# Optimization experiments

Hardware: AMD Instinct MI355X
Metric: run time of the kernel (lower is better)

Reference implementation:

```python
import jax, jax.numpy as jnp
import numpy as np

B, C, Hf, Wf = 32, 512, 16, 16
S = Hf * Wf            # 256 kv tokens
D = 2048               # d_model
DIN = 512              # d_input (attention embed dim)
HEADS = 8
DH = DIN // HEADS
T = 50                 # iterations (internal ticks)
M = 25                 # memory_length
HH = 16                # memory_hidden_dims
NSA = 512              # n_synch_action
NSO = 512              # n_synch_out
OUT = 1000             # out_dims


def _ln(x, g, b, eps=1e-5):
    mu = x.mean(-1, keepdims=True)
    var = ((x - mu) ** 2).mean(-1, keepdims=True)
    return (x - mu) / jnp.sqrt(var + eps) * g + b


def _glu(x):
    a, b = jnp.split(x, 2, axis=-1)
    return a * jax.nn.sigmoid(b)


def setup_inputs() -> dict:
    key = jax.random.key(0)
    ki = iter(jax.random.split(key, 40))
    def rn(shape, s=0.02):
        return jax.random.normal(next(ki), shape, jnp.float32) * s
    inp = {}
    inp['x'] = jax.random.normal(next(ki), (B, C, Hf, Wf), jnp.float32)
    # kv_proj: Linear(C->DIN) + LayerNorm
    inp['kv_w'] = rn((C, DIN)); inp['kv_b'] = jnp.zeros((DIN,), jnp.float32)
    inp['ln_kv_g'] = jnp.ones((DIN,), jnp.float32); inp['ln_kv_b'] = jnp.zeros((DIN,), jnp.float32)
    # q_proj: Linear(NSA->DIN)
    inp['q_w'] = rn((NSA, DIN)); inp['q_b'] = jnp.zeros((DIN,), jnp.float32)
    # MultiheadAttention projections
    inp['Wq'] = rn((DIN, DIN)); inp['bq'] = jnp.zeros((DIN,), jnp.float32)
    inp['Wk'] = rn((DIN, DIN)); inp['bk'] = jnp.zeros((DIN,), jnp.float32)
    inp['Wv'] = rn((DIN, DIN)); inp['bv'] = jnp.zeros((DIN,), jnp.float32)
    inp['Wo'] = rn((DIN, DIN)); inp['bo'] = jnp.zeros((DIN,), jnp.float32)
    # synapse: Linear(DIN+D -> 2D) + GLU + LayerNorm(D)
    inp['syn_w'] = rn((DIN + D, 2 * D)); inp['syn_b'] = jnp.zeros((2 * D,), jnp.float32)
    inp['ln_syn_g'] = jnp.ones((D,), jnp.float32); inp['ln_syn_b'] = jnp.zeros((D,), jnp.float32)
    # per-neuron NLMs (SuperLinear weights: (in,out,N))
    inp['nlm_w1'] = rn((M, 2 * HH, D), 0.1); inp['nlm_b1'] = jnp.zeros((1, D, 2 * HH), jnp.float32)
    inp['nlm_w2'] = rn((HH, 2, D), 0.1); inp['nlm_b2'] = jnp.zeros((1, D, 2), jnp.float32)
    # output projector
    inp['out_w'] = rn((NSO, OUT)); inp['out_b'] = jnp.zeros((OUT,), jnp.float32)
    # learnable decay params (clamped to [0,15] in forward)
    inp['decay_action'] = jax.random.uniform(next(ki), (NSA,), jnp.float32)
    inp['decay_out'] = jax.random.uniform(next(ki), (NSO,), jnp.float32)
    # learned start state
    inp['start_trace'] = rn((D, M), 0.05)
    inp['start_act'] = rn((D,), 0.05)
    # random-pairing neuron indices (fixed at init in the original)
    inp['idx_la'] = jax.random.randint(next(ki), (NSA,), 0, D)
    inp['idx_ra'] = jax.random.randint(next(ki), (NSA,), 0, D)
    inp['idx_lo'] = jax.random.randint(next(ki), (NSO,), 0, D)
    inp['idx_ro'] = jax.random.randint(next(ki), (NSO,), 0, D)
    return inp


def reference(x, kv_w, kv_b, ln_kv_g, ln_kv_b, q_w, q_b, Wq, bq, Wk, bk, Wv, bv, Wo, bo,
              syn_w, syn_b, ln_syn_g, ln_syn_b, nlm_w1, nlm_b1, nlm_w2, nlm_b2,
              out_w, out_b, decay_action, decay_out, start_trace, start_act,
              idx_la, idx_ra, idx_lo, idx_ro):
    # featurise: identity backbone, flatten spatial to tokens, project to DIN
    feats = x.reshape(B, C, S).transpose(0, 2, 1)                 # (B,S,C)
    kv = _ln(feats @ kv_w + kv_b, ln_kv_g, ln_kv_b)               # (B,S,DIN)
    kh = (kv @ Wk + bk).reshape(B, S, HEADS, DH).transpose(0, 2, 1, 3)  # (B,H,S,DH)
    vh = (kv @ Wv + bv).reshape(B, S, HEADS, DH).transpose(0, 2, 1, 3)
    r_a = jnp.exp(-jnp.clip(decay_action, 0.0, 15.0))[None]       # (1,NSA)
    r_o = jnp.exp(-jnp.clip(decay_out, 0.0, 15.0))[None]          # (1,NSO)

    def nlm(trace):  # per-neuron MLP over the memory axis: (B,D,M) -> (B,D)
        h = _glu(jnp.einsum('bdm,mhd->bdh', trace, nlm_w1) + nlm_b1)
        return _glu(jnp.einsum('bdh,hod->bdo', h, nlm_w2) + nlm_b2)[..., 0]

    act0 = jnp.broadcast_to(start_act[None], (B, D))
    trace0 = jnp.broadcast_to(start_trace[None], (B, D, M))
    # out-synchronisation initialised from the start state (before the loop)
    a_o0 = act0[:, idx_lo] * act0[:, idx_ro]
    b_o0 = jnp.ones_like(a_o0)
    a_a0 = jnp.zeros((B, NSA), jnp.float32)
    b_a0 = jnp.zeros((B, NSA), jnp.float32)
    log_out = jnp.log(jnp.float32(OUT))
    scale = 1.0 / jnp.sqrt(jnp.float32(DH))

    def step(carry, _):
        trace, act, a_a, b_a, a_o, b_o = carry
        # action synchronisation (decayed pairwise products, sync = alpha/sqrt(beta))
        a_a = r_a * a_a + act[:, idx_la] * act[:, idx_ra]
        b_a = r_a * b_a + 1.0
        sync_a = a_a / jnp.sqrt(b_a)
        # attention readout (single query token)
        q = sync_a @ q_w + q_b                                    # (B,DIN)
        qh = (q @ Wq + bq).reshape(B, HEADS, 1, DH)
        attn = jax.nn.softmax(jnp.einsum('bhqd,bhkd->bhqk', qh, kh) * scale, -1)
        o = jnp.einsum('bhqk,bhkd->bhqd', attn, vh).transpose(0, 2, 1, 3).reshape(B, DIN)
        attn_out = o @ Wo + bo
        # synapse MLP -> new pre-activation state
        pre = jnp.concatenate([attn_out, act], axis=-1)           # (B,DIN+D)
        state = _ln(_glu(pre @ syn_w + syn_b), ln_syn_g, ln_syn_b)
        trace = jnp.concatenate([trace[:, :, 1:], state[:, :, None]], axis=-1)
        act = nlm(trace)                                          # (B,D)
        # output synchronisation + prediction
        a_o = r_o * a_o + act[:, idx_lo] * act[:, idx_ro]
        b_o = r_o * b_o + 1.0
        sync_o = a_o / jnp.sqrt(b_o)
        pred = sync_o @ out_w + out_b                             # (B,OUT)
        logp = jax.nn.log_softmax(pred, -1)
        ne = -(jnp.exp(logp) * logp).sum(-1) / log_out
        cert = jnp.stack([ne, 1.0 - ne], axis=-1)                 # (B,2)
        return (trace, act, a_a, b_a, a_o, b_o), (pred, cert, sync_o)

    _, (preds, certs, syncs) = jax.lax.scan(step, (trace0, act0, a_a0, b_a0, a_o0, b_o0), None, length=T)
    predictions = jnp.transpose(preds, (1, 2, 0))                 # (B,OUT,T)
    certainties = jnp.transpose(certs, (1, 2, 0))                 # (B,2,T)
    return predictions, certainties, syncs[-1]
```

## Files before the change

kernel.cpp:

```cpp
#include <hip/hip_runtime.h>
#include <math.h>

#define BB 32
#define CC 512
#define SS 256
#define DD 2048
#define DIN 512
#define NH 8
#define DHD 64
#define TT 50
#define MM 25
#define HHID 16
#define NSA 512
#define NSO 512
#define NOUT 1000

__global__ void init_kernel(const float* __restrict__ dec_a, const float* __restrict__ dec_o,
                            const float* __restrict__ start_act, const float* __restrict__ start_trace,
                            const int* __restrict__ idx_lo, const int* __restrict__ idx_ro,
                            float* __restrict__ r_a, float* __restrict__ r_o,
                            float* __restrict__ a_a, float* __restrict__ b_a,
                            float* __restrict__ a_o, float* __restrict__ b_o,
                            float* __restrict__ trace)
{
    int i = blockIdx.x * 256 + threadIdx.x;
    if (i < 512) {
        r_a[i] = expf(-fminf(fmaxf(dec_a[i], 0.f), 15.f));
        r_o[i] = expf(-fminf(fmaxf(dec_o[i], 0.f), 15.f));
    }
    if (i < BB * NSA) {
        a_a[i] = 0.f; b_a[i] = 0.f;
        int j = i & 511;
        a_o[i] = start_act[idx_lo[j]] * start_act[idx_ro[j]];
        b_o[i] = 1.f;
    }
    if (i < BB * MM * DD) {
        int rem = i % (MM * DD);
        int m = rem / DD, d = rem % DD;
        trace[i] = start_trace[d * MM + m];
    }
}

template<int AMODE, int SMODE>
__global__ void gemm64(const float* __restrict__ A, const float* __restrict__ Bm,
                       const float* __restrict__ bias, float* __restrict__ Cm,
                       int Mdim, int Ndim, int Kdim)
{
    __shared__ float As[16 * 65];
    __shared__ float Bs[16 * 64];
    int row0 = blockIdx.x * 64;
    int col0 = blockIdx.y * 64;
    int t = threadIdx.x;
    int tx = t & 15, ty = t >> 4;
    float acc[4][4] = {};
    for (int k0 = 0; k0 < Kdim; k0 += 16) {
        if (AMODE == 0) {
            for (int i = t; i < 1024; i += 256) {
                int kk = i & 15, r = i >> 4;
                As[kk * 65 + r] = A[(size_t)(row0 + r) * Kdim + k0 + kk];
            }
        } else {
            int b = row0 / SS, s0 = row0 % SS;
            for (int i = t; i < 1024; i += 256) {
                int r = i & 63, kk = i >> 6;
// ... 46 lines not shown
    float v1 = buf[(size_t)row * 512 + 256 + t];
    red[t] = v0 + v1; __syncthreads();
    for (int off = 128; off; off >>= 1) { if (t < off) red[t] += red[t + off]; __syncthreads(); }
    float mu = red[0] * (1.f / 512.f); __syncthreads();
    float d0 = v0 - mu, d1 = v1 - mu;
    red[t] = d0 * d0 + d1 * d1; __syncthreads();
    for (int off = 128; off; off >>= 1) { if (t < off) red[t] += red[t + off]; __syncthreads(); }
    float rstd = 1.f / sqrtf(red[0] * (1.f / 512.f) + 1e-5f);
    buf[(size_t)row * 512 + t]       = d0 * rstd * g[t] + bta[t];
    buf[(size_t)row * 512 + 256 + t] = d1 * rstd * g[t + 256] + bta[t + 256];
}

__global__ void bqq_kernel(const float* __restrict__ q_b, const float* __restrict__ Wq,
                           const float* __restrict__ bq, float* __restrict__ bqq)
{
    int c = blockIdx.x * 256 + threadIdx.x;
    if (c >= 512) return;
    float acc = bq[c];
    for (int k = 0; k < 512; k++) acc += q_b[k] * Wq[k * 512 + c];
    bqq[c] = acc;
}

__global__ void bias2_kernel(const float* __restrict__ bo, const float* __restrict__ syn_w,
                             const float* __restrict__ syn_b, float* __restrict__ bias2)
{
    int c = blockIdx.x * 256 + threadIdx.x;
    if (c >= 4096) return;
    float acc = syn_b[c];
    for (int k = 0; k < 512; k++) acc += bo[k] * syn_w[(size_t)k * 4096 + c];
    bias2[c] = acc;
}

__global__ void wt_build(const float* __restrict__ W2, const float* __restrict__ syn_w,
                         float* __restrict__ WT)
{
    __shared__ float tile[32][33];
    int k0 = blockIdx.x * 32, c0 = blockIdx.y * 32;
    int t = threadIdx.x;
    int col = t & 31, rq = t >> 5;
    #pragma unroll
    for (int q = 0; q < 4; ++q) {
        int kk = q * 8 + rq;
        int k = k0 + kk;
        const float* src = (k < 512 ? W2 : syn_w) + (size_t)k * 4096 + c0;
        tile[kk][col] = src[col];
    }
    __syncthreads();
    #pragma unroll
    for (int q = 0; q < 4; ++q) {
        int cc = q * 8 + rq;
        WT[(size_t)(c0 + cc) * 2560 + k0 + col] = tile[col][cc];
    }
}

__global__ void act0_kernel(const float* __restrict__ start_act, float* __restrict__ act0slot)
{
    int i = blockIdx.x * 256 + threadIdx.x;
    if (i < BB * DD) act0slot[i] = start_act[i & (DD - 1)];
}

__global__ void pad_outw(const float* __restrict__ out_w, const float* __restrict__ out_b,
                         float* __restrict__ out_wp, float* __restrict__ out_bp)
{
    int i = blockIdx.x * 256 + threadIdx.x;
    if (i < 512 * 1024) {
        int r = i >> 10, c = i & 1023;
        out_wp[i] = (c < 1000) ? out_w[r * 1000 + c] : 0.f;
    }
    if (i < 1024) out_bp[i] = (i < 1000) ? out_b[i] : 0.f;
}

__global__ __launch_bounds__(256) void k1_front(
    const float* __restrict__ act, const int* __restrict__ la, const int* __restrict__ ra,
    const float* __restrict__ r_a,
    const float* __restrict__ aold, const float* __restrict__ bold,
    float* __restrict__ anew, float* __restrict__ bnew,
    const float* __restrict__ Wqq, const float* __restrict__ bqq,
    const float* __restrict__ khT, const float* __restrict__ vh,
    float* __restrict__ obuf)
{
    __shared__ float sa[512];
    __shared__ float qp[256];
    __shared__ float qs[64];
    __shared__ float ps[256];
    __shared__ float red[256];
    int bh = blockIdx.x, b = bh >> 3, h = bh & 7;
    int tid = threadIdx.x;
    const float* actb = act + b * DD;
    for (int j = tid; j < 512; j += 256) {
        float p = actb[la[j]] * actb[ra[j]];
        float r = r_a[j];
        float aa = r * aold[b * 512 + j] + p;
        float bb = r * bold[b * 512 + j] + 1.f;
        sa[j] = aa / sqrtf(bb);
        if (h == 0) { anew[b * 512 + j] = aa; bnew[b * 512 + j] = bb; }
    }
    __syncthreads();
    {
        int cl = tid & 63, q = tid >> 6;
        const float* wcol = Wqq + h * 64 + cl;
        float acc = 0.f;
        #pragma unroll 8
        for (int k = q * 128; k < q * 128 + 128; ++k)
            acc += sa[k] * wcol[k * 512];
        qp[tid] = acc;
    }
    __syncthreads();
    if (tid < 64)
        qs[tid] = qp[tid] + qp[tid + 64] + qp[tid + 128] + qp[tid + 192] + bqq[h * 64 + tid];
    __syncthreads();
    const float* kb = khT + (size_t)bh * 64 * 256;
    float sc = 0.f;
    #pragma unroll 8
    for (int dh = 0; dh < 64; ++dh) sc += qs[dh] * kb[dh * 256 + tid];
    sc *= 0.125f;
    red[tid] = sc; __syncthreads();
    for (int off = 128; off; off >>= 1) { if (tid < off) red[tid] = fmaxf(red[tid], red[tid + off]); __syncthreads(); }
    float mx = red[0]; __syncthreads();
    float e = expf(sc - mx);
    red[tid] = e; __syncthreads();
    for (int off = 128; off; off >>= 1) { if (tid < off) red[tid] += red[tid + off]; __syncthreads(); }
    float inv = 1.f / red[0];
    ps[tid] = e * inv;
    __syncthreads();
    int dh = tid & 63, ch = tid >> 6;
    const float* vb = vh + (size_t)bh * 256 * 64;
    float acc = 0.f;
    for (int s = ch * 64; s < ch * 64 + 64; ++s) acc += ps[s] * vb[s * 64 + dh];
    red[tid] = acc; __syncthreads();
    if (tid < 128) red[tid] += red[tid + 128];
    __syncthreads();
    if (tid < 64) obuf[b * 512 + h * 64 + tid] = red[tid] + red[tid + 64];
}

__global__ __launch_bounds__(256) void k2_glu(
    const float* __restrict__ obuf, const float* __restrict__ act,
    const float* __restrict__ WT, const float* __restrict__ bias2,
    float* __restrict__ glbufT, float* __restrict__ partials)
{
    __shared__ float As[2 * 32 * 160];
    int tid = threadIdx.x, blk = blockIdx.x;
    int kh = tid >> 7;
    int cpair = (tid >> 5) & 3;
    int r = tid & 31;
    int c = blk * 4 + cpair;
    const float* wta = WT + (size_t)c * 2560 + kh * 1280;
    const float* wtb = WT + (size_t)(c + 2048) * 2560 + kh * 1280;
    float acc_a = 0.f, acc_b = 0.f;
    for (int ri = 0; ri < 8; ++ri) {
        __syncthreads();
        #pragma unroll
        for (int q = 0; q < 10; ++q) {
            int i = tid + q * 256;
            int hh = i / 1280;
            int rem = i - hh * 1280;
            int rr = rem / 40, kg = rem - (rem / 40) * 40;
            int k = hh * 1280 + ri * 160 + kg * 4;
            float4 v;
            if (k < 512) v = *(const float4*)(obuf + rr * 512 + k);
            else         v = *(const float4*)(act + rr * 2048 + (k - 512));
            *(float4*)(As + hh * 5120 + rr * 160 + ((kg ^ (rr & 7)) << 2)) = v;
        }
        __syncthreads();
        const float* Ar = As + kh * 5120 + r * 160;
        const float* wtaa = wta + ri * 160;
        const float* wtbb = wtb + ri * 160;
        int sw = r & 7;
        #pragma unroll 8
        for (int kc = 0; kc < 40; ++kc) {
            float4 a4 = *(const float4*)(Ar + ((kc ^ sw) << 2));
            float4 wa = *(const float4*)(wtaa + kc * 4);
            float4 wb = *(const float4*)(wtbb + kc * 4);
            acc_a += a4.x * wa.x + a4.y * wa.y + a4.z * wa.z + a4.w * wa.w;
            acc_b += a4.x * wb.x + a4.y * wb.y + a4.z * wb.z + a4.w * wb.w;
        }
    }
    __syncthreads();
    float* red_a = As;
    float* red_b = As + 128;
    float* gls   = As + 256;
    float* gl2s  = As + 384;
    if (kh == 1) {
        red_a[cpair * 32 + r] = acc_a;
        red_b[cpair * 32 + r] = acc_b;
    }
    __syncthreads();
    if (kh == 0) {
        float ua = acc_a + red_a[cpair * 32 + r] + bias2[c];
        float ub = acc_b + red_b[cpair * 32 + r] + bias2[c + 2048];
        float gl = ua * (1.f / (1.f + expf(-ub)));
        glbufT[c * 32 + r] = gl;
        gls[cpair * 32 + r] = gl;
        gl2s[cpair * 32 + r] = gl * gl;
    }
    __syncthreads();
    if (tid < 32) {
        float s = 0.f, s2 = 0.f;
        #pragma unroll
        for (int cp = 0; cp < 4; ++cp) { s += gls[cp * 32 + tid]; s2 += gl2s[cp * 32 + tid]; }
        partials[blk * 64 + tid * 2]     = s;
        partials[blk * 64 + tid * 2 + 1] = s2;
    }
}

#define K4_LDS_FLOATS (12800 + 2176 + 256 + 256 + 16)
__global__ __launch_bounds__(256) void k4_nlm(
    const float* __restrict__ glbufT, const float* __restrict__ partials,
    const float* __restrict__ g, const float* __restrict__ bta,
    float* __restrict__ trace,
    const float* __restrict__ w1, const float* __restrict__ b1,
    const float* __restrict__ w2, const float* __restrict__ b2,
    float* __restrict__ actout, int t_iter)
{
    extern __shared__ float lds[];
    float* wlds  = lds;
    float* cross = lds + 12800;
    float* r1 = lds + 14976;
    float* r2 = lds + 15232;
    float* sm = lds + 15488;
    int tid = threadIdx.x, blk = blockIdx.x;
    int dtile = blk & 127, bgrp = blk >> 7;
    int d0 = dtile * 16, b0 = bgrp * 8;
    int hh = tid >> 7;
    int b_l = (tid >> 4) & 7;
    int d_l = tid & 15;
    int b = b0 + b_l, d = d0 + d_l;

    for (int q = 0; q < 50; ++q) {
        int i = tid + q * 256;
        wlds[i] = w1[(size_t)(i >> 4) * 2048 + d0 + (i & 15)];
    }
    {
        int bb = tid >> 5, j = tid & 31;
        int bstat = b0 + bb;
        float s = 0.f, s2 = 0.f;
        #pragma unroll
        for (int q = 0; q < 16; ++q) {
            int kblk = j + 32 * q;
            s  += partials[kblk * 64 + bstat * 2];
            s2 += partials[kblk * 64 + bstat * 2 + 1];
        }
        r1[tid] = s; r2[tid] = s2;
        __syncthreads();
        for (int off = 16; off; off >>= 1) {
            if (j < off) { r1[tid] += r1[tid + off]; r2[tid] += r2[tid + off]; }
            __syncthreads();
        }
        if (j == 0) {
            float mu = r1[tid] * (1.f / 2048.f);
            float var = r2[tid] * (1.f / 2048.f) - mu * mu;
            sm[bb * 2] = mu;
            sm[bb * 2 + 1] = 1.f / sqrtf(var + 1e-5f);
        }
        __syncthreads();
    }
    float mu = sm[b_l * 2], rstd = sm[b_l * 2 + 1];
    float gl = glbufT[d * 32 + b];
    float nv = (gl - mu) * rstd * g[d] + bta[d];
    int newrow = t_iter % MM;
    if (hh == 0) trace[((size_t)b * MM + newrow) * DD + d] = nv;

    float hp[16];
    {
        const float* b1d = b1 + d * 32 + hh * 16;
        #pragma unroll
        for (int h = 0; h < 16; h++) hp[h] = b1d[h];
    }
    const float* trb = trace + (size_t)b * MM * DD + d;
    for (int m = 0; m < 24; m++) {
        int mph = (t_iter + 1 + m) % 25;
        float tv = trb[(size_t)mph * DD];
        const float* wm = wlds + (m * 32 + hh * 16) * 16 + d_l;
        #pragma unroll
        for (int h = 0; h < 16; h++) hp[h] += tv * wm[h * 16];
    }
    {
        const float* wm = wlds + (24 * 32 + hh * 16) * 16 + d_l;
        #pragma unroll
        for (int h = 0; h < 16; h++) hp[h] += nv * wm[h * 16];
    }
    if (hh == 1) {
        float* cx = cross + (b_l * 16 + d_l) * 17;
        #pragma unroll
        for (int h = 0; h < 16; h++) cx[h] = hp[h];
    }
    __syncthreads();
    if (hh == 0) {
        const float* cx = cross + (b_l * 16 + d_l) * 17;
        float o0 = b2[d * 2], o1 = b2[d * 2 + 1];
        #pragma unroll
        for (int h = 0; h < 16; h++) {
            float hv = hp[h] * (1.f / (1.f + expf(-cx[h])));
            o0 += hv * w2[((size_t)h * 2) * DD + d];
            o1 += hv * w2[((size_t)h * 2 + 1) * DD + d];
        }
        actout[b * DD + d] = o0 * (1.f / (1.f + expf(-o1)));
    }
}

__global__ __launch_bounds__(256) void k_syncscan(
    const float* __restrict__ acthist, const int* __restrict__ lo, const int* __restrict__ ro,
    const float* __restrict__ r_o,
    const float* __restrict__ a_o0, const float* __restrict__ b_o0,
    float* __restrict__ so_hist, float* __restrict__ out_sync)
{
    int idx = blockIdx.x * 256 + threadIdx.x;
    int b = idx >> 9, j = idx & 511;
    float aa = a_o0[idx], bb = b_o0[idx];
    float rr = r_o[j];
    int il = lo[j], ir = ro[j];
    const float* ah = acthist + (size_t)(BB * DD) + b * DD;
    float s = 0.f;
    for (int t = 0; t < TT; ++t) {
        float p = ah[il] * ah[ir];
        aa = rr * aa + p;
        bb = rr * bb + 1.f;
        s = aa / sqrtf(bb);
        so_hist[(size_t)t * (BB * 512) + idx] = s;
        ah += BB * DD;
    }
    out_sync[idx] = s;
}

__global__ __launch_bounds__(256) void k6_cert(
    const float* __restrict__ predt, float* __restrict__ d_out)
{
    int t_iter = blockIdx.x >> 5, b = blockIdx.x & 31, t = threadIdx.x;
    __shared__ float red[256];
    const float* pr = predt + ((size_t)t_iter * 32 + b) * 1024;
// ... 42 lines not shown
    const float* kv_b     = (const float*)d_in[2];
    const float* ln_kv_g  = (const float*)d_in[3];
    const float* ln_kv_b  = (const float*)d_in[4];
    const float* q_w      = (const float*)d_in[5];
    const float* q_b      = (const float*)d_in[6];
    const float* Wq       = (const float*)d_in[7];
    const float* bq       = (const float*)d_in[8];
    const float* Wk       = (const float*)d_in[9];
    const float* bk       = (const float*)d_in[10];
    const float* Wv       = (const float*)d_in[11];
    const float* bv       = (const float*)d_in[12];
    const float* Wo       = (const float*)d_in[13];
    const float* bo       = (const float*)d_in[14];
    const float* syn_w    = (const float*)d_in[15];
    const float* syn_b    = (const float*)d_in[16];
    const float* ln_syn_g = (const float*)d_in[17];
    const float* ln_syn_b = (const float*)d_in[18];
    const float* nlm_w1   = (const float*)d_in[19];
    const float* nlm_b1   = (const float*)d_in[20];
    const float* nlm_w2   = (const float*)d_in[21];
    const float* nlm_b2   = (const float*)d_in[22];
    const float* out_w    = (const float*)d_in[23];
    const float* out_b    = (const float*)d_in[24];
    const float* dec_a    = (const float*)d_in[25];
    const float* dec_o    = (const float*)d_in[26];
    const float* start_tr = (const float*)d_in[27];
    const float* start_ac = (const float*)d_in[28];
    const int*   idx_la   = (const int*)d_in[29];
    const int*   idx_ra   = (const int*)d_in[30];
    const int*   idx_lo   = (const int*)d_in[31];
    const int*   idx_ro   = (const int*)d_in[32];
    float* out = (float*)d_out;

    float* w = (float*)d_ws;
    float* kvbuf = w;            w += (size_t)8192 * 512;
    float* khT   = w;            w += (size_t)8192 * 512;
    float* vhb   = w;            w += (size_t)8192 * 512;
    float* Wqq   = w;            w += (size_t)512 * 512;
    float* bqq   = w;            w += 512;
    float* W2    = w;            w += (size_t)512 * 4096;
    float* WT    = w;            w += (size_t)4096 * 2560;
    float* bias2 = w;            w += 4096;
    float* r_a   = w;            w += 512;
    float* r_o   = w;            w += 512;
    float* a_a   = w;            w += 2 * BB * NSA;
    float* b_a   = w;            w += 2 * BB * NSA;
    float* a_o   = w;            w += BB * NSO;
    float* b_o   = w;            w += BB * NSO;
    float* trace = w;            w += (size_t)BB * MM * DD;
    float* obuf  = w;            w += BB * DIN;
    float* glbufT = w;           w += (size_t)DD * BB;
    float* partials = w;         w += 512 * 32 * 2;

    float* acthist = kvbuf;
    float* so_hist = vhb;
    float* out_wp  = khT;
    float* out_bp  = khT + 524288;
    float* predt   = W2;

    init_kernel<<<6400, 256, 0, stream>>>(dec_a, dec_o, start_ac, start_tr, idx_lo, idx_ro,
                                          r_a, r_o, a_a, b_a, a_o, b_o, trace);
    gemm64<1, 0><<<dim3(128, 8), 256, 0, stream>>>(x, kv_w, kv_b, kvbuf, 8192, 512, 512);
    ln_rows<<<8192, 256, 0, stream>>>(kvbuf, ln_kv_g, ln_kv_b);
    gemm64<0, 1><<<dim3(128, 8), 256, 0, stream>>>(kvbuf, Wk, bk, khT, 8192, 512, 512);
    gemm64<0, 2><<<dim3(128, 8), 256, 0, stream>>>(kvbuf, Wv, bv, vhb, 8192, 512, 512);
    gemm64<0, 0><<<dim3(8, 8), 256, 0, stream>>>(q_w, Wq, nullptr, Wqq, 512, 512, 512);
    bqq_kernel<<<2, 256, 0, stream>>>(q_b, Wq, bq, bqq);
    gemm64<0, 0><<<dim3(8, 64), 256, 0, stream>>>(Wo, syn_w, nullptr, W2, 512, 4096, 512);
    bias2_kernel<<<16, 256, 0, stream>>>(bo, syn_w, syn_b, bias2);
    wt_build<<<dim3(80, 128), 256, 0, stream>>>(W2, syn_w, WT);
    act0_kernel<<<256, 256, 0, stream>>>(start_ac, acthist);

    float* out_sync = out + (size_t)BB * NOUT * TT + (size_t)BB * 2 * TT;

    static int lds_attr_set = 0;
    if (!lds_attr_set) {
        hipFuncSetAttribute(reinterpret_cast<const void*>(k4_nlm),
                            hipFuncAttributeMaxDynamicSharedMemorySize,
                            K4_LDS_FLOATS * 4);
        lds_attr_set = 1;
    }

    for (int t = 0; t < TT; ++t) {
        int par = t & 1;
        const float* act_t = acthist + (size_t)t * (BB * DD);
        float* act_n = acthist + (size_t)(t + 1) * (BB * DD);
        k1_front<<<256, 256, 0, stream>>>(act_t, idx_la, idx_ra, r_a,
                                          a_a + par * (BB * 512), b_a + par * (BB * 512),
                                          a_a + (par ^ 1) * (BB * 512), b_a + (par ^ 1) * (BB * 512),
                                          Wqq, bqq, khT, vhb, obuf);
        k2_glu<<<512, 256, 0, stream>>>(obuf, act_t, WT, bias2, glbufT, partials);
        k4_nlm<<<512, 256, K4_LDS_FLOATS * 4, stream>>>(glbufT, partials,
                                            ln_syn_g, ln_syn_b, trace,
                                            nlm_w1, nlm_b1, nlm_w2, nlm_b2, act_n, t);
    }

    k_syncscan<<<64, 256, 0, stream>>>(acthist, idx_lo, idx_ro, r_o, a_o, b_o,
                                       so_hist, out_sync);
    pad_outw<<<2048, 256, 0, stream>>>(out_w, out_b, out_wp, out_bp);
    gemm64<0, 0><<<dim3(25, 16), 256, 0, stream>>>(so_hist, out_wp, out_bp, predt,
                                                   1600, 1024, 512);
    k6_cert<<<1600, 256, 0, stream>>>(predt, out);
}
```

Baseline: 5.039 ms.

## Fuse per-tick kernels into one persistent kernel with grid barriers

The three kernels launched per tick over 50 ticks are replaced by a single persistent kernel of 256 blocks x 512 threads. It walks all ticks and separates the attention, GLU and NLM phases with atomic-counter grid barriers. The NLM first-layer weights are loaded into LDS once per block, and per-tick buffers are kept in ring or history slots to avoid races across barriers. This removes about 150 launch gaps and the repeated weight staging. In exchange it relies on all 256 blocks being co-resident, since the spin barrier deadlocks otherwise, and it uses relaxed atomics whose memory ordering is fragile.

```diff
diff --git a/kernel.cpp b/kernel.cpp
--- a/kernel.cpp
+++ b/kernel.cpp
@@ -15,21 +15,37 @@
 #define NSO 512
 #define NOUT 1000
 
+#define NBLK 256
+#define BLKT 512
+
+#define WL_FLOATS 25600
+#define SCR_OFF   25600
+#define LDS_FLOATS (25600 + 10240)
+
+__device__ __forceinline__ float cld(const float* p) {
+    return __hip_atomic_load(p, __ATOMIC_RELAXED, __HIP_MEMORY_SCOPE_AGENT);
+}
+__device__ __forceinline__ void cst(float* p, float v) {
+    __hip_atomic_store(p, v, __ATOMIC_RELAXED, __HIP_MEMORY_SCOPE_AGENT);
+}
+
 __global__ void init_kernel(const float* __restrict__ dec_a, const float* __restrict__ dec_o,
                             const float* __restrict__ start_act, const float* __restrict__ start_trace,
                             const int* __restrict__ idx_lo, const int* __restrict__ idx_ro,
+                            unsigned* __restrict__ bar,
                             float* __restrict__ r_a, float* __restrict__ r_o,
-                            float* __restrict__ a_a, float* __restrict__ b_a,
+                            float* __restrict__ aslot0, float* __restrict__ bslot0,
                             float* __restrict__ a_o, float* __restrict__ b_o,
                             float* __restrict__ trace)
 {
     int i = blockIdx.x * 256 + threadIdx.x;
+    if (i < 16) bar[i] = 0u;
     if (i < 512) {
         r_a[i] = expf(-fminf(fmaxf(dec_a[i], 0.f), 15.f));
         r_o[i] = expf(-fminf(fmaxf(dec_o[i], 0.f), 15.f));
     }
     if (i < BB * NSA) {
-        a_a[i] = 0.f; b_a[i] = 0.f;
+        aslot0[i] = 0.f; bslot0[i] = 0.f;
         int j = i & 511;
         a_o[i] = start_act[idx_lo[j]] * start_act[idx_ro[j]];
         b_o[i] = 1.f;
@@ -180,231 +196,275 @@
     if (i < 1024) out_bp[i] = (i < 1000) ? out_b[i] : 0.f;
 }
 
-__global__ __launch_bounds__(256) void k1_front(
-    const float* __restrict__ act, const int* __restrict__ la, const int* __restrict__ ra,
-    const float* __restrict__ r_a,
-    const float* __restrict__ aold, const float* __restrict__ bold,
-    float* __restrict__ anew, float* __restrict__ bnew,
-    const float* __restrict__ Wqq, const float* __restrict__ bqq,
-    const float* __restrict__ khT, const float* __restrict__ vh,
-    float* __restrict__ obuf)
-{
-    __shared__ float sa[512];
-    __shared__ float qp[256];
-    __shared__ float qs[64];
-    __shared__ float ps[256];
-    __shared__ float red[256];
-    int bh = blockIdx.x, b = bh >> 3, h = bh & 7;
-    int tid = threadIdx.x;
-    const float* actb = act + b * DD;
-    for (int j = tid; j < 512; j += 256) {
-        float p = actb[la[j]] * actb[ra[j]];
-        float r = r_a[j];
-        float aa = r * aold[b * 512 + j] + p;
-        float bb = r * bold[b * 512 + j] + 1.f;
-        sa[j] = aa / sqrtf(bb);
-        if (h == 0) { anew[b * 512 + j] = aa; bnew[b * 512 + j] = bb; }
-    }
+__device__ __forceinline__ void gsync(unsigned* __restrict__ ctr, unsigned target)
+{
+    __threadfence_block();
     __syncthreads();
+    if (threadIdx.x == 0) {
+        __hip_atomic_fetch_add(ctr, 1u, __ATOMIC_RELAXED, __HIP_MEMORY_SCOPE_AGENT);
+        while (__hip_atomic_load(ctr, __ATOMIC_RELAXED, __HIP_MEMORY_SCOPE_AGENT) < target)
+            __builtin_amdgcn_s_sleep(4);
+        asm volatile("" ::: "memory");
+    }
+    __syncthreads();
+}
+
+struct PArgs {
+    const float* Wqq; const float* bqq;
+    const float* khT; const float* vh;
+    const float* WT;  const float* bias2;
+    const float* g_syn; const float* bt_syn;
+    const float* w1; const float* b1; const float* w2; const float* b2;
+    const float* r_a;
+    const int* la; const int* ra;
+    float* aslot; float* bslot;
+    float* acthist;
+    float* trace;
+    float* obufR;
+    float* glbuf;
+    float* partR;
+    unsigned* bar;
+};
+
+__global__ __launch_bounds__(BLKT) void tick_kernel(PArgs A)
+{
+    extern __shared__ float lds[];
+    float* wlds = lds;
+    float* scr  = lds + SCR_OFF;
+    const int blk = blockIdx.x;
+    const int tid = threadIdx.x;
+    unsigned nb = 0;
+
     {
-        int cl = tid & 63, q = tid >> 6;
-        const float* wcol = Wqq + h * 64 + cl;
-        float acc = 0.f;
-        #pragma unroll 8
-        for (int k = q * 128; k < q * 128 + 128; ++k)
-            acc += sa[k] * wcol[k * 512];
-        qp[tid] = acc;
-    }
-    __syncthreads();
-    if (tid < 64)
-        qs[tid] = qp[tid] + qp[tid + 64] + qp[tid + 128] + qp[tid + 192] + bqq[h * 64 + tid];
-    __syncthreads();
-    const float* kb = khT + (size_t)bh * 64 * 256;
-    float sc = 0.f;
-    #pragma unroll 8
-    for (int dh = 0; dh < 64; ++dh) sc += qs[dh] * kb[dh * 256 + tid];
-    sc *= 0.125f;
-    red[tid] = sc; __syncthreads();
-    for (int off = 128; off; off >>= 1) { if (tid < off) red[tid] = fmaxf(red[tid], red[tid + off]); __syncthreads(); }
-    float mx = red[0]; __syncthreads();
-    float e = expf(sc - mx);
-    red[tid] = e; __syncthreads();
-    for (int off = 128; off; off >>= 1) { if (tid < off) red[tid] += red[tid + off]; __syncthreads(); }
-    float inv = 1.f / red[0];
-    ps[tid] = e * inv;
-    __syncthreads();
-    int dh = tid & 63, ch = tid >> 6;
-    const float* vb = vh + (size_t)bh * 256 * 64;
-    float acc = 0.f;
-    for (int s = ch * 64; s < ch * 64 + 64; ++s) acc += ps[s] * vb[s * 64 + dh];
-    red[tid] = acc; __syncthreads();
-    if (tid < 128) red[tid] += red[tid + 128];
-    __syncthreads();
-    if (tid < 64) obuf[b * 512 + h * 64 + tid] = red[tid] + red[tid + 64];
-}
-
-__global__ __launch_bounds__(256) void k2_glu(
-    const float* __restrict__ obuf, const float* __restrict__ act,
-    const float* __restrict__ WT, const float* __restrict__ bias2,
-    float* __restrict__ glbufT, float* __restrict__ partials)
-{
-    __shared__ float As[2 * 32 * 160];
-    int tid = threadIdx.x, blk = blockIdx.x;
-    int kh = tid >> 7;
-    int cpair = (tid >> 5) & 3;
-    int r = tid & 31;
-    int c = blk * 4 + cpair;
-    const float* wta = WT + (size_t)c * 2560 + kh * 1280;
-    const float* wtb = WT + (size_t)(c + 2048) * 2560 + kh * 1280;
-    float acc_a = 0.f, acc_b = 0.f;
-    for (int ri = 0; ri < 8; ++ri) {
+        int d0 = (blk & 63) * 32;
+        for (int q = 0; q < 50; ++q) {
+            int i = tid + q * BLKT;
+            wlds[i] = A.w1[(size_t)(i >> 5) * 2048 + d0 + (i & 31)];
+        }
         __syncthreads();
-        #pragma unroll
-        for (int q = 0; q < 10; ++q) {
-            int i = tid + q * 256;
-            int hh = i / 1280;
-            int rem = i - hh * 1280;
-            int rr = rem / 40, kg = rem - (rem / 40) * 40;
-            int k = hh * 1280 + ri * 160 + kg * 4;
-            float4 v;
-            if (k < 512) v = *(const float4*)(obuf + rr * 512 + k);
-            else         v = *(const float4*)(act + rr * 2048 + (k - 512));
-            *(float4*)(As + hh * 5120 + rr * 160 + ((kg ^ (rr & 7)) << 2)) = v;
-        }
-        __syncthreads();
-        const float* Ar = As + kh * 5120 + r * 160;
-        const float* wtaa = wta + ri * 160;
-        const float* wtbb = wtb + ri * 160;
-        int sw = r & 7;
-        #pragma unroll 8
-        for (int kc = 0; kc < 40; ++kc) {
-            float4 a4 = *(const float4*)(Ar + ((kc ^ sw) << 2));
-            float4 wa = *(const float4*)(wtaa + kc * 4);
-            float4 wb = *(const float4*)(wtbb + kc * 4);
-            acc_a += a4.x * wa.x + a4.y * wa.y + a4.z * wa.z + a4.w * wa.w;
-            acc_b += a4.x * wb.x + a4.y * wb.y + a4.z * wb.z + a4.w * wb.w;
-        }
-    }
-    __syncthreads();
-    float* red_a = As;
-    float* red_b = As + 128;
-    float* gls   = As + 256;
-    float* gl2s  = As + 384;
-    if (kh == 1) {
-        red_a[cpair * 32 + r] = acc_a;
-        red_b[cpair * 32 + r] = acc_b;
-    }
-    __syncthreads();
-    if (kh == 0) {
-        float ua = acc_a + red_a[cpair * 32 + r] + bias2[c];
-        float ub = acc_b + red_b[cpair * 32 + r] + bias2[c + 2048];
-        float gl = ua * (1.f / (1.f + expf(-ub)));
-        glbufT[c * 32 + r] = gl;
-        gls[cpair * 32 + r] = gl;
-        gl2s[cpair * 32 + r] = gl * gl;
-    }
-    __syncthreads();
-    if (tid < 32) {
-        float s = 0.f, s2 = 0.f;
-        #pragma unroll
-        for (int cp = 0; cp < 4; ++cp) { s += gls[cp * 32 + tid]; s2 += gl2s[cp * 32 + tid]; }
-        partials[blk * 64 + tid * 2]     = s;
-        partials[blk * 64 + tid * 2 + 1] = s2;
-    }
-}
-
-#define K4_LDS_FLOATS (12800 + 2176 + 256 + 256 + 16)
-__global__ __launch_bounds__(256) void k4_nlm(
-    const float* __restrict__ glbufT, const float* __restrict__ partials,
-    const float* __restrict__ g, const float* __restrict__ bta,
-    float* __restrict__ trace,
-    const float* __restrict__ w1, const float* __restrict__ b1,
-    const float* __restrict__ w2, const float* __restrict__ b2,
-    float* __restrict__ actout, int t_iter)
-{
-    extern __shared__ float lds[];
-    float* wlds  = lds;
-    float* cross = lds + 12800;
-    float* r1 = lds + 14976;
-    float* r2 = lds + 15232;
-    float* sm = lds + 15488;
-    int tid = threadIdx.x, blk = blockIdx.x;
-    int dtile = blk & 127, bgrp = blk >> 7;
-    int d0 = dtile * 16, b0 = bgrp * 8;
-    int hh = tid >> 7;
-    int b_l = (tid >> 4) & 7;
-    int d_l = tid & 15;
-    int b = b0 + b_l, d = d0 + d_l;
-
-    for (int q = 0; q < 50; ++q) {
-        int i = tid + q * 256;
-        wlds[i] = w1[(size_t)(i >> 4) * 2048 + d0 + (i & 15)];
-    }
-    {
-        int bb = tid >> 5, j = tid & 31;
-        int bstat = b0 + bb;
-        float s = 0.f, s2 = 0.f;
-        #pragma unroll
-        for (int q = 0; q < 16; ++q) {
-            int kblk = j + 32 * q;
-            s  += partials[kblk * 64 + bstat * 2];
-            s2 += partials[kblk * 64 + bstat * 2 + 1];
-        }
-        r1[tid] = s; r2[tid] = s2;
-        __syncthreads();
-        for (int off = 16; off; off >>= 1) {
-            if (j < off) { r1[tid] += r1[tid + off]; r2[tid] += r2[tid + off]; }
-            __syncthreads();
-        }
-        if (j == 0) {
-            float mu = r1[tid] * (1.f / 2048.f);
-            float var = r2[tid] * (1.f / 2048.f) - mu * mu;
-            sm[bb * 2] = mu;
-            sm[bb * 2 + 1] = 1.f / sqrtf(var + 1e-5f);
-        }
-        __syncthreads();
-    }
-    float mu = sm[b_l * 2], rstd = sm[b_l * 2 + 1];
-    float gl = glbufT[d * 32 + b];
-    float nv = (gl - mu) * rstd * g[d] + bta[d];
-    int newrow = t_iter % MM;
-    if (hh == 0) trace[((size_t)b * MM + newrow) * DD + d] = nv;
-
-    float hp[16];
-    {
-        const float* b1d = b1 + d * 32 + hh * 16;
-        #pragma unroll
-        for (int h = 0; h < 16; h++) hp[h] = b1d[h];
-    }
-    const float* trb = trace + (size_t)b * MM * DD + d;
-    for (int m = 0; m < 24; m++) {
-        int mph = (t_iter + 1 + m) % 25;
-        float tv = trb[(size_t)mph * DD];
-        const float* wm = wlds + (m * 32 + hh * 16) * 16 + d_l;
-        #pragma unroll
-        for (int h = 0; h < 16; h++) hp[h] += tv * wm[h * 16];
-    }
-    {
-        const float* wm = wlds + (24 * 32 + hh * 16) * 16 + d_l;
-        #pragma unroll
-        for (int h = 0; h < 16; h++) hp[h] += nv * wm[h * 16];
-    }
-    if (hh == 1) {
-        float* cx = cross + (b_l * 16 + d_l) * 17;
-        #pragma unroll
-        for (int h = 0; h < 16; h++) cx[h] = hp[h];
-    }
-    __syncthreads();
-    if (hh == 0) {
-        const float* cx = cross + (b_l * 16 + d_l) * 17;
-        float o0 = b2[d * 2], o1 = b2[d * 2 + 1];
-        #pragma unroll
-        for (int h = 0; h < 16; h++) {
-            float hv = hp[h] * (1.f / (1.f + expf(-cx[h])));
-            o0 += hv * w2[((size_t)h * 2) * DD + d];
-            o1 += hv * w2[((size_t)h * 2 + 1) * DD + d];
-        }
-        actout[b * DD + d] = o0 * (1.f / (1.f + expf(-o1)));
+    }
+
+    for (int t = 0; t < TT; ++t) {
+        const float* act_t = A.acthist + (size_t)t * (BB * DD);
+        float* obuf_t = A.obufR + (size_t)t * (BB * DIN);
+        float* part_t = A.partR + (size_t)t * (256 * 64);
+
+        {
+            int b = blk >> 3, h = blk & 7;
+            float* sa  = scr;
+            float* qp  = scr + 512;
+            float* qs  = scr + 1024;
+            float* ps  = scr + 1088;
+            float* red = scr + 1344;
+            const float* as_t = A.aslot + (size_t)t * (BB * 512);
+            const float* bs_t = A.bslot + (size_t)t * (BB * 512);
+            float* as_n = A.aslot + (size_t)(t + 1) * (BB * 512);
+            float* bs_n = A.bslot + (size_t)(t + 1) * (BB * 512);
+            const float* actb = act_t + b * DD;
+            {
+                int j = tid;
+                float p = actb[A.la[j]] * actb[A.ra[j]];
+                float r = A.r_a[j];
+                float aa = r * as_t[b * 512 + j] + p;
+                float bb = r * bs_t[b * 512 + j] + 1.f;
+                sa[j] = aa / sqrtf(bb);
+                if (h == 0) { cst(&as_n[b * 512 + j], aa); cst(&bs_n[b * 512 + j], bb); }
+            }
+            __syncthreads();
+            {
+                int cl = tid & 63, q = tid >> 6;
+                const float* wcol = A.Wqq + h * 64 + cl;
+                float acc = 0.f;
+                #pragma unroll 8
+                for (int k = q * 64; k < q * 64 + 64; ++k)
+                    acc += sa[k] * wcol[k * 512];
+                qp[tid] = acc;
+            }
+            __syncthreads();
+            if (tid < 64) {
+                float s = A.bqq[h * 64 + tid];
+                #pragma unroll
+                for (int i = 0; i < 8; ++i) s += qp[tid + 64 * i];
+                qs[tid] = s;
+            }
+            __syncthreads();
+            float sc = 0.f;
+            if (tid < 256) {
+                const float* kb = A.khT + (size_t)blk * 16384;
+                #pragma unroll 8
+                for (int dh = 0; dh < 64; ++dh) sc += qs[dh] * kb[dh * 256 + tid];
+                sc *= 0.125f;
+            }
+            red[tid] = (tid < 256) ? sc : -1e30f;
+            __syncthreads();
+            for (int off = 256; off; off >>= 1) { if (tid < off) red[tid] = fmaxf(red[tid], red[tid + off]); __syncthreads(); }
+            float mx = red[0]; __syncthreads();
+            float e = (tid < 256) ? expf(sc - mx) : 0.f;
+            red[tid] = e; __syncthreads();
+            for (int off = 256; off; off >>= 1) { if (tid < off) red[tid] += red[tid + off]; __syncthreads(); }
+            float inv = 1.f / red[0];
+            if (tid < 256) ps[tid] = e * inv;
+            __syncthreads();
+            {
+                int dh = tid & 63, ch = tid >> 6;
+                const float* vb = A.vh + (size_t)blk * 16384;
+                float acc = 0.f;
+                #pragma unroll
+                for (int s = ch * 32; s < ch * 32 + 32; ++s) acc += ps[s] * vb[s * 64 + dh];
+                red[tid] = acc; __syncthreads();
+                if (tid < 256) red[tid] += red[tid + 256]; __syncthreads();
+                if (tid < 128) red[tid] += red[tid + 128]; __syncthreads();
+                if (tid < 64) cst(&obuf_t[b * 512 + h * 64 + tid], red[tid] + red[tid + 64]);
+            }
+        }
+        nb += NBLK; gsync(A.bar, nb);
+
+        {
+            float* As = scr;
+            int kh = tid >> 8;
+            int cpair = (tid >> 5) & 7;
+            int r = tid & 31;
+            int c = blk * 8 + cpair;
+            const float* wta = A.WT + (size_t)c * 2560 + kh * 1280;
+            const float* wtb = A.WT + (size_t)(c + 2048) * 2560 + kh * 1280;
+            float acc_a = 0.f, acc_b = 0.f;
+            for (int ri = 0; ri < 8; ++ri) {
+                __syncthreads();
+                #pragma unroll
+                for (int q = 0; q < 5; ++q) {
+                    int i = tid + q * BLKT;
+                    int hh2 = i / 1280;
+                    int rem = i - hh2 * 1280;
+                    int rr = rem / 40, kg = rem - (rem / 40) * 40;
+                    int k = hh2 * 1280 + ri * 160 + kg * 4;
+                    float4 v;
+                    if (k < 512) v = *(const float4*)(obuf_t + rr * 512 + k);
+                    else         v = *(const float4*)(act_t + rr * 2048 + (k - 512));
+                    *(float4*)(As + hh2 * 5120 + rr * 160 + ((kg ^ (rr & 7)) << 2)) = v;
+                }
+                __syncthreads();
+                const float* Ar = As + kh * 5120 + r * 160;
+                const float* wtaa = wta + ri * 160;
+                const float* wtbb = wtb + ri * 160;
+                int sw = r & 7;
+                #pragma unroll 8
+                for (int kc = 0; kc < 40; ++kc) {
+                    float4 a4 = *(const float4*)(Ar + ((kc ^ sw) << 2));
+                    float4 wa = *(const float4*)(wtaa + kc * 4);
+                    float4 wb = *(const float4*)(wtbb + kc * 4);
+                    acc_a += a4.x * wa.x + a4.y * wa.y + a4.z * wa.z + a4.w * wa.w;
+                    acc_b += a4.x * wb.x + a4.y * wb.y + a4.z * wb.z + a4.w * wb.w;
+                }
+            }
+            __syncthreads();
+            float* red_a = scr;
+            float* red_b = scr + 256;
+            float* gls   = scr + 512;
+            float* gl2s  = scr + 768;
+            if (kh == 1) {
+                red_a[cpair * 32 + r] = acc_a;
+                red_b[cpair * 32 + r] = acc_b;
+            }
+            __syncthreads();
+            if (kh == 0) {
+                float ua = acc_a + red_a[cpair * 32 + r] + A.bias2[c];
+                float ub = acc_b + red_b[cpair * 32 + r] + A.bias2[c + 2048];
+                float gl = ua * (1.f / (1.f + expf(-ub)));
+                cst(&A.glbuf[c * 32 + r], gl);
+                gls[cpair * 32 + r] = gl;
+                gl2s[cpair * 32 + r] = gl * gl;
+            }
+            __syncthreads();
+            if (tid < 32) {
+                float s = 0.f, s2 = 0.f;
+                #pragma unroll
+                for (int cp = 0; cp < 8; ++cp) { s += gls[cp * 32 + tid]; s2 += gl2s[cp * 32 + tid]; }
+                cst(&part_t[blk * 64 + tid * 2], s);
+                cst(&part_t[blk * 64 + tid * 2 + 1], s2);
+            }
+        }
+        nb += NBLK; gsync(A.bar, nb);
+
+        {
+            int dtile = blk & 63, bgrp = blk >> 6;
+            int d0 = dtile * 32, b0 = bgrp * 8;
+            int hh = tid >> 8;
+            int b_l = (tid >> 5) & 7;
+            int d_l = tid & 31;
+            int b = b0 + b_l, d = d0 + d_l;
+            float* cross = scr;
+            float* r1 = scr + 4352;
+            float* r2 = scr + 4864;
+            float* sm = scr + 5376;
+            {
+                int bb = tid >> 6;
+                int j = tid & 63;
+                int bstat = b0 + bb;
+                float s = 0.f, s2 = 0.f;
+                #pragma unroll
+                for (int q = 0; q < 4; ++q) {
+                    int kblk = j + 64 * q;
+                    s  += part_t[kblk * 64 + bstat * 2];
+                    s2 += part_t[kblk * 64 + bstat * 2 + 1];
+                }
+                r1[tid] = s; r2[tid] = s2;
+                __syncthreads();
+                for (int off = 32; off; off >>= 1) {
+                    if (j < off) { r1[tid] += r1[tid + off]; r2[tid] += r2[tid + off]; }
+                    __syncthreads();
+                }
+                if (j == 0) {
+                    float mu = r1[tid] * (1.f / 2048.f);
+                    float var = r2[tid] * (1.f / 2048.f) - mu * mu;
+                    sm[bb * 2] = mu;
+                    sm[bb * 2 + 1] = 1.f / sqrtf(var + 1e-5f);
+                }
+                __syncthreads();
+            }
+            float mu = sm[b_l * 2], rstd = sm[b_l * 2 + 1];
+            float gl = cld(&A.glbuf[d * 32 + b]);
+            float nv = (gl - mu) * rstd * A.g_syn[d] + A.bt_syn[d];
+            int newrow = t % MM;
+            if (hh == 0) A.trace[((size_t)b * MM + newrow) * DD + d] = nv;
+            float hp[16];
+            {
+                const float* b1d = A.b1 + d * 32 + hh * 16;
+                #pragma unroll
+                for (int h = 0; h < 16; h++) hp[h] = b1d[h];
+            }
+            const float* trb = A.trace + (size_t)b * MM * DD + d;
+            for (int m = 0; m < 24; m++) {
+                int mph = (t + 1 + m) % 25;
+                float tv = trb[(size_t)mph * DD];
+                const float* wm = wlds + (m * 32 + hh * 16) * 32 + d_l;
+                #pragma unroll
+                for (int h = 0; h < 16; h++) hp[h] += tv * wm[h * 32];
+            }
+            {
+                const float* wm = wlds + (24 * 32 + hh * 16) * 32 + d_l;
+                #pragma unroll
+                for (int h = 0; h < 16; h++) hp[h] += nv * wm[h * 32];
+            }
+            if (hh == 1) {
+                float* cx = cross + (b_l * 32 + d_l) * 17;
+                #pragma unroll
+                for (int h = 0; h < 16; h++) cx[h] = hp[h];
+            }
+            __syncthreads();
+            if (hh == 0) {
+                const float* cx = cross + (b_l * 32 + d_l) * 17;
+                float o0 = A.b2[d * 2], o1 = A.b2[d * 2 + 1];
+                #pragma unroll
+                for (int h = 0; h < 16; h++) {
+                    float hv = hp[h] * (1.f / (1.f + expf(-cx[h])));
+                    o0 += hv * A.w2[((size_t)h * 2) * DD + d];
+                    o1 += hv * A.w2[((size_t)h * 2 + 1) * DD + d];
+                }
+                cst(&A.acthist[(size_t)(t + 1) * (BB * DD) + b * DD + d],
+                    o0 * (1.f / (1.f + expf(-o1))));
+            }
+        }
+        nb += NBLK; gsync(A.bar, nb);
     }
 }
 
@@ -513,7 +573,8 @@
     const int*   idx_ro   = (const int*)d_in[32];
     float* out = (float*)d_out;
 
-    float* w = (float*)d_ws;
+    unsigned* bar = (unsigned*)d_ws;
+    float* w = (float*)d_ws + 64;
     float* kvbuf = w;            w += (size_t)8192 * 512;
     float* khT   = w;            w += (size_t)8192 * 512;
     float* vhb   = w;            w += (size_t)8192 * 512;
@@ -524,23 +585,23 @@
     float* bias2 = w;            w += 4096;
     float* r_a   = w;            w += 512;
     float* r_o   = w;            w += 512;
-    float* a_a   = w;            w += 2 * BB * NSA;
-    float* b_a   = w;            w += 2 * BB * NSA;
     float* a_o   = w;            w += BB * NSO;
     float* b_o   = w;            w += BB * NSO;
     float* trace = w;            w += (size_t)BB * MM * DD;
-    float* obuf  = w;            w += BB * DIN;
-    float* glbufT = w;           w += (size_t)DD * BB;
-    float* partials = w;         w += 512 * 32 * 2;
+    float* glbuf = w;            w += (size_t)DD * BB;
+    float* aslot = w;            w += (size_t)(TT + 1) * BB * 512;
+    float* bslot = w;            w += (size_t)(TT + 1) * BB * 512;
 
     float* acthist = kvbuf;
+    float* obufR   = W2;
+    float* partR   = W2 + 819200;
     float* so_hist = vhb;
+    float* predt   = vhb + 819200;
     float* out_wp  = khT;
     float* out_bp  = khT + 524288;
-    float* predt   = W2;
 
     init_kernel<<<6400, 256, 0, stream>>>(dec_a, dec_o, start_ac, start_tr, idx_lo, idx_ro,
-                                          r_a, r_o, a_a, b_a, a_o, b_o, trace);
+                                          bar, r_a, r_o, aslot, bslot, a_o, b_o, trace);
     gemm64<1, 0><<<dim3(128, 8), 256, 0, stream>>>(x, kv_w, kv_b, kvbuf, 8192, 512, 512);
     ln_rows<<<8192, 256, 0, stream>>>(kvbuf, ln_kv_g, ln_kv_b);
     gemm64<0, 1><<<dim3(128, 8), 256, 0, stream>>>(kvbuf, Wk, bk, khT, 8192, 512, 512);
@@ -556,25 +617,25 @@
 
     static int lds_attr_set = 0;
     if (!lds_attr_set) {
-        hipFuncSetAttribute(reinterpret_cast<const void*>(k4_nlm),
+        hipFuncSetAttribute(reinterpret_cast<const void*>(tick_kernel),
                             hipFuncAttributeMaxDynamicSharedMemorySize,
-                            K4_LDS_FLOATS * 4);
+                            LDS_FLOATS * 4);
         lds_attr_set = 1;
     }
 
-    for (int t = 0; t < TT; ++t) {
-        int par = t & 1;
-        const float* act_t = acthist + (size_t)t * (BB * DD);
-        float* act_n = acthist + (size_t)(t + 1) * (BB * DD);
-        k1_front<<<256, 256, 0, stream>>>(act_t, idx_la, idx_ra, r_a,
-                                          a_a + par * (BB * 512), b_a + par * (BB * 512),
-                                          a_a + (par ^ 1) * (BB * 512), b_a + (par ^ 1) * (BB * 512),
-                                          Wqq, bqq, khT, vhb, obuf);
-        k2_glu<<<512, 256, 0, stream>>>(obuf, act_t, WT, bias2, glbufT, partials);
-        k4_nlm<<<512, 256, K4_LDS_FLOATS * 4, stream>>>(glbufT, partials,
-                                            ln_syn_g, ln_syn_b, trace,
-                                            nlm_w1, nlm_b1, nlm_w2, nlm_b2, act_n, t);
-    }
+    PArgs pa;
+    pa.Wqq = Wqq; pa.bqq = bqq;
+    pa.khT = khT; pa.vh = vhb;
+    pa.WT = WT; pa.bias2 = bias2;
+    pa.g_syn = ln_syn_g; pa.bt_syn = ln_syn_b;
+    pa.w1 = nlm_w1; pa.b1 = nlm_b1; pa.w2 = nlm_w2; pa.b2 = nlm_b2;
+    pa.r_a = r_a;
+    pa.la = idx_la; pa.ra = idx_ra;
+    pa.aslot = aslot; pa.bslot = bslot;
+    pa.acthist = acthist; pa.trace = trace;
+    pa.obufR = obufR; pa.glbuf = glbuf; pa.partR = partR;
+    pa.bar = bar;
+    tick_kernel<<<NBLK, BLKT, LDS_FLOATS * 4, stream>>>(pa);
 
     k_syncscan<<<64, 256, 0, stream>>>(acthist, idx_lo, idx_ro, r_o, a_o, b_o,
                                        so_hist, out_sync);
```

Result: slower. 8.227 ms (+63.3%).

## Store per-step weights and K/V in bf16 to halve memory traffic

Applied to the files above, without the earlier changes.

Converts the fused synapse weight matrix, the per-head K and V tensors, and the NLM first-layer weights to bf16 once, before the 50-iteration loop. The per-step kernels then read half the bytes and unpack to fp32 for accumulation, with k2's inner loop reworked to consume 8 bf16 values per 16-byte load. The loop kernels are bound by streaming these large weights from memory each tick, so halving bytes should cut per-step time. The cost is an extra conversion kernel, buffer reshuffling, and reduced precision in the weights, K and V, which could affect accuracy tolerances.

```diff
diff --git a/kernel.cpp b/kernel.cpp
--- a/kernel.cpp
+++ b/kernel.cpp
@@ -14,6 +14,21 @@
 #define NSA 512
 #define NSO 512
 #define NOUT 1000
+
+__device__ __forceinline__ unsigned short f2bf(float f) {
+    unsigned u = __float_as_uint(f);
+    u += 0x7fffu + ((u >> 16) & 1u);
+    return (unsigned short)(u >> 16);
+}
+__device__ __forceinline__ float bf2f(unsigned short s) {
+    return __uint_as_float((unsigned)s << 16);
+}
+__device__ __forceinline__ float blo(unsigned u) {
+    return __uint_as_float(u << 16);
+}
+__device__ __forceinline__ float bhi(unsigned u) {
+    return __uint_as_float(u & 0xffff0000u);
+}
 
 __global__ void init_kernel(const float* __restrict__ dec_a, const float* __restrict__ dec_o,
                             const float* __restrict__ start_act, const float* __restrict__ start_trace,
@@ -142,7 +157,7 @@
 }
 
 __global__ void wt_build(const float* __restrict__ W2, const float* __restrict__ syn_w,
-                         float* __restrict__ WT)
+                         unsigned short* __restrict__ WTh)
 {
     __shared__ float tile[32][33];
     int k0 = blockIdx.x * 32, c0 = blockIdx.y * 32;
@@ -159,8 +174,19 @@
     #pragma unroll
     for (int q = 0; q < 4; ++q) {
         int cc = q * 8 + rq;
-        WT[(size_t)(c0 + cc) * 2560 + k0 + col] = tile[col][cc];
-    }
+        WTh[(size_t)(c0 + cc) * 2560 + k0 + col] = f2bf(tile[col][cc]);
+    }
+}
+
+__global__ void conv_kernel(const float* __restrict__ khT, const float* __restrict__ vh,
+                            const float* __restrict__ w1,
+                            unsigned short* __restrict__ khTh, unsigned short* __restrict__ vhh,
+                            unsigned short* __restrict__ w1h)
+{
+    int i = blockIdx.x * 256 + threadIdx.x;
+    khTh[i] = f2bf(khT[i]);
+    vhh[i]  = f2bf(vh[i]);
+    if (i < 25 * 32 * DD) w1h[i] = f2bf(w1[i]);
 }
 
 __global__ void act0_kernel(const float* __restrict__ start_act, float* __restrict__ act0slot)
@@ -186,7 +212,7 @@
     const float* __restrict__ aold, const float* __restrict__ bold,
     float* __restrict__ anew, float* __restrict__ bnew,
     const float* __restrict__ Wqq, const float* __restrict__ bqq,
-    const float* __restrict__ khT, const float* __restrict__ vh,
+    const unsigned short* __restrict__ khTh, const unsigned short* __restrict__ vhh,
     float* __restrict__ obuf)
 {
     __shared__ float sa[512];
@@ -219,10 +245,10 @@
     if (tid < 64)
         qs[tid] = qp[tid] + qp[tid + 64] + qp[tid + 128] + qp[tid + 192] + bqq[h * 64 + tid];
     __syncthreads();
-    const float* kb = khT + (size_t)bh * 64 * 256;
+    const unsigned short* kb = khTh + (size_t)bh * 64 * 256;
     float sc = 0.f;
     #pragma unroll 8
-    for (int dh = 0; dh < 64; ++dh) sc += qs[dh] * kb[dh * 256 + tid];
+    for (int dh = 0; dh < 64; ++dh) sc += qs[dh] * bf2f(kb[dh * 256 + tid]);
     sc *= 0.125f;
     red[tid] = sc; __syncthreads();
     for (int off = 128; off; off >>= 1) { if (tid < off) red[tid] = fmaxf(red[tid], red[tid + off]); __syncthreads(); }
@@ -234,9 +260,9 @@
     ps[tid] = e * inv;
     __syncthreads();
     int dh = tid & 63, ch = tid >> 6;
-    const float* vb = vh + (size_t)bh * 256 * 64;
+    const unsigned short* vb = vhh + (size_t)bh * 256 * 64;
     float acc = 0.f;
-    for (int s = ch * 64; s < ch * 64 + 64; ++s) acc += ps[s] * vb[s * 64 + dh];
+    for (int s = ch * 64; s < ch * 64 + 64; ++s) acc += ps[s] * bf2f(vb[s * 64 + dh]);
     red[tid] = acc; __syncthreads();
     if (tid < 128) red[tid] += red[tid + 128];
     __syncthreads();
@@ -245,7 +271,7 @@
 
 __global__ __launch_bounds__(256) void k2_glu(
     const float* __restrict__ obuf, const float* __restrict__ act,
-    const float* __restrict__ WT, const float* __restrict__ bias2,
+    const unsigned short* __restrict__ WTh, const float* __restrict__ bias2,
     float* __restrict__ glbufT, float* __restrict__ partials)
 {
     __shared__ float As[2 * 32 * 160];
@@ -254,8 +280,8 @@
     int cpair = (tid >> 5) & 3;
     int r = tid & 31;
     int c = blk * 4 + cpair;
-    const float* wta = WT + (size_t)c * 2560 + kh * 1280;
-    const float* wtb = WT + (size_t)(c + 2048) * 2560 + kh * 1280;
+    const unsigned short* wta = WTh + (size_t)c * 2560 + kh * 1280;
+    const unsigned short* wtb = WTh + (size_t)(c + 2048) * 2560 + kh * 1280;
     float acc_a = 0.f, acc_b = 0.f;
     for (int ri = 0; ri < 8; ++ri) {
         __syncthreads();
@@ -273,16 +299,19 @@
         }
         __syncthreads();
         const float* Ar = As + kh * 5120 + r * 160;
-        const float* wtaa = wta + ri * 160;
-        const float* wtbb = wtb + ri * 160;
+        const unsigned short* wtaa = wta + ri * 160;
+        const unsigned short* wtbb = wtb + ri * 160;
         int sw = r & 7;
-        #pragma unroll 8
-        for (int kc = 0; kc < 40; ++kc) {
-            float4 a4 = *(const float4*)(Ar + ((kc ^ sw) << 2));
-            float4 wa = *(const float4*)(wtaa + kc * 4);
-            float4 wb = *(const float4*)(wtbb + kc * 4);
-            acc_a += a4.x * wa.x + a4.y * wa.y + a4.z * wa.z + a4.w * wa.w;
-            acc_b += a4.x * wb.x + a4.y * wb.y + a4.z * wb.z + a4.w * wb.w;
+        #pragma unroll 4
+        for (int kc = 0; kc < 20; ++kc) {
+            uint4 wa = *(const uint4*)(wtaa + kc * 8);
+            uint4 wb = *(const uint4*)(wtbb + kc * 8);
+            float4 a0 = *(const float4*)(Ar + (((2 * kc) ^ sw) << 2));
+            float4 a1 = *(const float4*)(Ar + (((2 * kc + 1) ^ sw) << 2));
+            acc_a += a0.x * blo(wa.x) + a0.y * bhi(wa.x) + a0.z * blo(wa.y) + a0.w * bhi(wa.y)
+                   + a1.x * blo(wa.z) + a1.y * bhi(wa.z) + a1.z * blo(wa.w) + a1.w * bhi(wa.w);
+            acc_b += a0.x * blo(wb.x) + a0.y * bhi(wb.x) + a0.z * blo(wb.y) + a0.w * bhi(wb.y)
+                   + a1.x * blo(wb.z) + a1.y * bhi(wb.z) + a1.z * blo(wb.w) + a1.w * bhi(wb.w);
         }
     }
     __syncthreads();
@@ -318,7 +347,7 @@
     const float* __restrict__ glbufT, const float* __restrict__ partials,
     const float* __restrict__ g, const float* __restrict__ bta,
     float* __restrict__ trace,
-    const float* __restrict__ w1, const float* __restrict__ b1,
+    const unsigned short* __restrict__ w1h, const float* __restrict__ b1,
     const float* __restrict__ w2, const float* __restrict__ b2,
     float* __restrict__ actout, int t_iter)
 {
@@ -338,7 +367,7 @@
 
     for (int q = 0; q < 50; ++q) {
         int i = tid + q * 256;
-        wlds[i] = w1[(size_t)(i >> 4) * 2048 + d0 + (i & 15)];
+        wlds[i] = bf2f(w1h[(size_t)(i >> 4) * 2048 + d0 + (i & 15)]);
     }
     {
         int bb = tid >> 5, j = tid & 31;
@@ -520,7 +549,6 @@
     float* Wqq   = w;            w += (size_t)512 * 512;
     float* bqq   = w;            w += 512;
     float* W2    = w;            w += (size_t)512 * 4096;
-    float* WT    = w;            w += (size_t)4096 * 2560;
     float* bias2 = w;            w += 4096;
     float* r_a   = w;            w += 512;
     float* r_o   = w;            w += 512;
@@ -532,12 +560,16 @@
     float* obuf  = w;            w += BB * DIN;
     float* glbufT = w;           w += (size_t)DD * BB;
     float* partials = w;         w += 512 * 32 * 2;
+    unsigned short* WTh  = (unsigned short*)w;  w += (size_t)4096 * 2560 / 2;
+    unsigned short* khTh = (unsigned short*)w;  w += (size_t)8192 * 512 / 2;
+    unsigned short* vhh  = (unsigned short*)w;  w += (size_t)8192 * 512 / 2;
+    unsigned short* w1h  = (unsigned short*)w;  w += (size_t)25 * 32 * DD / 2;
 
     float* acthist = kvbuf;
     float* so_hist = vhb;
+    float* predt   = vhb + 819200;
     float* out_wp  = khT;
     float* out_bp  = khT + 524288;
-    float* predt   = W2;
 
     init_kernel<<<6400, 256, 0, stream>>>(dec_a, dec_o, start_ac, start_tr, idx_lo, idx_ro,
                                           r_a, r_o, a_a, b_a, a_o, b_o, trace);
@@ -549,7 +581,8 @@
     bqq_kernel<<<2, 256, 0, stream>>>(q_b, Wq, bq, bqq);
     gemm64<0, 0><<<dim3(8, 64), 256, 0, stream>>>(Wo, syn_w, nullptr, W2, 512, 4096, 512);
     bias2_kernel<<<16, 256, 0, stream>>>(bo, syn_w, syn_b, bias2);
-    wt_build<<<dim3(80, 128), 256, 0, stream>>>(W2, syn_w, WT);
+    wt_build<<<dim3(80, 128), 256, 0, stream>>>(W2, syn_w, WTh);
+    conv_kernel<<<16384, 256, 0, stream>>>(khT, vhb, nlm_w1, khTh, vhh, w1h);
     act0_kernel<<<256, 256, 0, stream>>>(start_ac, acthist);
 
     float* out_sync = out + (size_t)BB * NOUT * TT + (size_t)BB * 2 * TT;
@@ -569,11 +602,11 @@
         k1_front<<<256, 256, 0, stream>>>(act_t, idx_la, idx_ra, r_a,
                                           a_a + par * (BB * 512), b_a + par * (BB * 512),
                                           a_a + (par ^ 1) * (BB * 512), b_a + (par ^ 1) * (BB * 512),
-                                          Wqq, bqq, khT, vhb, obuf);
-        k2_glu<<<512, 256, 0, stream>>>(obuf, act_t, WT, bias2, glbufT, partials);
+                                          Wqq, bqq, khTh, vhh, obuf);
+        k2_glu<<<512, 256, 0, stream>>>(obuf, act_t, WTh, bias2, glbufT, partials);
         k4_nlm<<<512, 256, K4_LDS_FLOATS * 4, stream>>>(glbufT, partials,
                                             ln_syn_g, ln_syn_b, trace,
-                                            nlm_w1, nlm_b1, nlm_w2, nlm_b2, act_n, t);
+                                            w1h, nlm_b1, nlm_w2, nlm_b2, act_n, t);
     }
 
     k_syncscan<<<64, 256, 0, stream>>>(acthist, idx_lo, idx_ro, r_o, a_o, b_o,
```

Result: faster. 4.405 ms (-12.6%).
